# Kernel tuning notes

Measured on AMD Instinct MI355X. Metric: run time of the kernel, lower is better.

Reference implementation:

```python
import jax, jax.numpy as jnp
import numpy as np

DIM_IN, DIM_Q, DIM_K = 1024, 128, 128
B, S = 8, 2048

def setup_inputs() -> dict:
    key = jax.random.key(0)
    ks = jax.random.split(key, 9)
    sq = 1.0 / np.sqrt(DIM_IN)
    return {
        "query": jax.random.normal(ks[0], (B, S, DIM_IN), jnp.float32),
        "key": jax.random.normal(ks[1], (B, S, DIM_IN), jnp.float32),
        "value": jax.random.normal(ks[2], (B, S, DIM_IN), jnp.float32),
        "Wq": jax.random.uniform(ks[3], (DIM_IN, DIM_Q), jnp.float32, -sq, sq),
        "bq": jax.random.uniform(ks[4], (DIM_Q,), jnp.float32, -sq, sq),
        "Wk": jax.random.uniform(ks[5], (DIM_IN, DIM_K), jnp.float32, -sq, sq),
        "bk": jax.random.uniform(ks[6], (DIM_K,), jnp.float32, -sq, sq),
        "Wv": jax.random.uniform(ks[7], (DIM_IN, DIM_K), jnp.float32, -sq, sq),
        "bv": jax.random.uniform(ks[8], (DIM_K,), jnp.float32, -sq, sq),
    }

def reference(query, key, value, Wq, bq, Wk, bk, Wv, bv):
    q = jnp.einsum("bsd,dq->bsq", query, Wq) + bq          # [B,S,Dq]
    k = jnp.einsum("bsd,dk->bsk", key, Wk) + bk            # [B,S,Dk]
    v = jnp.einsum("bsd,dk->bsk", value, Wv) + bv          # [B,S,Dk]
    scale = jnp.asarray(q.shape[-1] ** 0.5, q.dtype)
    scores = jnp.einsum("bqd,bkd->bqk", q, k) / scale      # [B,S,S]
    attn = jax.nn.softmax(scores, axis=-1)
    return jnp.einsum("bqk,bkd->bqd", attn, v)             # [B,S,Dk]
```

## Files before the change

### kernel.cpp

```cpp
#include <hip/hip_runtime.h>

typedef __attribute__((ext_vector_type(8))) short short8;
typedef __attribute__((ext_vector_type(4))) float floatx4;

#define MFMA16(a, b, c) __builtin_amdgcn_mfma_f32_16x16x32_bf16(a, b, c, 0, 0, 0)

__device__ __forceinline__ short f2bf(float f) {
    unsigned int u = __float_as_uint(f);
    u = u + 0x7fffu + ((u >> 16) & 1u);
    return (short)(u >> 16);
}

__device__ __forceinline__ void ldst16(const void* g, void* l) {
    __builtin_amdgcn_global_load_lds(
        (const __attribute__((address_space(1))) void*)g,
        (__attribute__((address_space(3))) void*)l, 16, 0, 0);
}

__global__ __launch_bounds__(256) void wconv_kernel(const float* __restrict__ Wq,
                                                    const float* __restrict__ Wk,
                                                    const float* __restrict__ Wv,
                                                    short* __restrict__ wt) {
    int idx = blockIdx.x * 256 + threadIdx.x;
    int w = idx >> 17;
    int rem = idx & 131071;
    int k = rem >> 7, n = rem & 127;
    const float* W = (w == 0) ? Wq : (w == 1) ? Wk : Wv;
    wt[w * 131072 + n * 1024 + k] = f2bf(W[rem]);
}

__global__ __launch_bounds__(256, 3) void proj_kernel(const float* __restrict__ Q,
                                                      const float* __restrict__ K,
                                                      const float* __restrict__ V,
                                                      const short* __restrict__ wt,
                                                      const float* __restrict__ bq,
                                                      const float* __restrict__ bk,
                                                      const float* __restrict__ bv,
                                                      short* __restrict__ qo,
                                                      short* __restrict__ ko,
                                                      short* __restrict__ vo) {
    alignas(16) __shared__ float Asl[64 * 64];
    alignas(16) __shared__ short Wsl[128 * 64];
    const int t = threadIdx.x;
    const int wv = t >> 6, L = t & 63;
    const int q4 = L >> 4, l16 = L & 15;
    const int which = blockIdx.y;
    const float* A = (which == 0) ? Q : (which == 1) ? K : V;
    const short* Wt = wt + which * 131072;
    const float* bias = (which == 0) ? bq : (which == 1) ? bk : bv;
    const int m0 = blockIdx.x * 64;
    const int mw = m0 + 16 * wv;

    floatx4 acc[8];
    for (int nt = 0; nt < 8; nt++) acc[nt] = (floatx4)0.0f;

    for (int k0 = 0; k0 < 1024; k0 += 64) {
        __syncthreads();
        for (int j = 0; j < 4; j++) {
            int s = (4 * wv + j) * 64 + L;
            int r = s >> 4, p = s & 15, c = p ^ (r & 15);
            ldst16(A + (size_t)(m0 + r) * 1024 + k0 + c * 4,
                   Asl + (4 * wv + j) * 256);
        }
        for (int j = 0; j < 4; j++) {
            int s = (4 * wv + j) * 64 + L;
            int r = s >> 3, p = s & 7, c = p ^ (r & 7);
            ldst16(Wt + (size_t)r * 1024 + k0 + c * 8,
                   Wsl + (4 * wv + j) * 512);
        }
        __syncthreads();

        for (int ks = 0; ks < 2; ks++) {
            int c0 = 8 * ks + 2 * q4;
            const int ar = 16 * wv + l16;
            float4 f0 = *(float4*)&Asl[ar * 64 + (c0 ^ l16) * 4];
            float4 f1 = *(float4*)&Asl[ar * 64 + ((c0 + 1) ^ l16) * 4];
            short8 af;
            af[0] = f2bf(f0.x); af[1] = f2bf(f0.y); af[2] = f2bf(f0.z); af[3] = f2bf(f0.w);
            af[4] = f2bf(f1.x); af[5] = f2bf(f1.y); af[6] = f2bf(f1.z); af[7] = f2bf(f1.w);
            int cw = 4 * ks + q4;
            for (int nt = 0; nt < 8; nt++) {
                int wr = 16 * nt + l16;
                short8 bf = *(short8*)&Wsl[wr * 64 + (cw ^ (l16 & 7)) * 8];
                acc[nt] = MFMA16(af, bf, acc[nt]);
            }
        }
    }

    for (int nt = 0; nt < 8; nt++) {
        float bvv = bias[16 * nt + l16];
        for (int r = 0; r < 4; r++) {
            float val = acc[nt][r] + bvv;
            short h = f2bf(val);
            int grow = mw + q4 * 4 + r;
            int col = 16 * nt + l16;
            if (which == 0) {
                qo[(size_t)grow * 128 + col] = h;
            } else if (which == 1) {
                ko[(size_t)grow * 128 + col] = h;
            } else {
                int bb = grow >> 11, s = grow & 2047;
                vo[(size_t)bb * 262144 + (size_t)col * 2048 + s] = h;
            }
        }
    }
}

__global__ __launch_bounds__(256, 2) void flash_kernel(const short* __restrict__ qw,
                                                       const short* __restrict__ kw,
                                                       const short* __restrict__ vw,
                                                       float* __restrict__ out) {
    alignas(16) __shared__ short Kl[2][64][136];
    alignas(16) __shared__ short Vl[2][128][72];
    alignas(16) __shared__ short Pl[2][32][72];
    const int t = threadIdx.x;
    const int wv = t >> 6, L = t & 63;
    const int pr = wv >> 1, wq = wv & 1;
    const int pt = t & 127;
    const int q4 = L >> 4, l16 = L & 15;
    const int bq = blockIdx.x, b = blockIdx.y;
    const short* qp = qw + (size_t)b * 262144 + (size_t)bq * 32 * 128;
    const short* kp = kw + (size_t)b * 262144;
    const short* vp = vw + (size_t)b * 262144;

    short8 qf[4];
    for (int ks = 0; ks < 4; ks++)
        qf[ks] = *(const short8*)(qp + (16 * wq + l16) * 128 + ks * 32 + q4 * 8);

    floatx4 oacc[8];
    for (int dt = 0; dt < 8; dt++) oacc[dt] = (floatx4)0.0f;
    float m_i[4] = {-1e30f, -1e30f, -1e30f, -1e30f};
    float l_i[4] = {0.f, 0.f, 0.f, 0.f};
    const float SL = (float)(0.08838834764831845 * 1.4426950408889634);

    for (int kt = 0; kt < 16; kt++) {
        const int kv0 = (pr * 16 + kt) * 64;
        __syncthreads();
        for (int j = 0; j < 8; j++) {
            int flat = j * 128 + pt;
            int row = flat >> 4, c16 = flat & 15;
            *(short8*)&Kl[pr][row][c16 * 8] = *(const short8*)(kp + (size_t)(kv0 + row) * 128 + c16 * 8);
        }
        for (int j = 0; j < 8; j++) {
            int flat = j * 128 + pt;
            int row = flat >> 3, c8 = flat & 7;
            *(short8*)&Vl[pr][row][c8 * 8] = *(const short8*)(vp + (size_t)row * 2048 + kv0 + c8 * 8);
        }
        __syncthreads();

        floatx4 sa[4];
        for (int nt = 0; nt < 4; nt++) {
            sa[nt] = (floatx4)0.0f;
            for (int ks = 0; ks < 4; ks++) {
                short8 bfr = *(short8*)&Kl[pr][16 * nt + l16][ks * 32 + q4 * 8];
                sa[nt] = MFMA16(qf[ks], bfr, sa[nt]);
            }
        }

        float p[4][4], mnew[4], alpha[4];
        for (int r = 0; r < 4; r++) {
            float mx = fmaxf(fmaxf(sa[0][r], sa[1][r]), fmaxf(sa[2][r], sa[3][r]));
            mx *= SL;
            for (int off = 8; off >= 1; off >>= 1) mx = fmaxf(mx, __shfl_xor(mx, off, 64));
            mnew[r] = fmaxf(m_i[r], mx);
            alpha[r] = __builtin_amdgcn_exp2f(m_i[r] - mnew[r]);
            float rs = 0.f;
            for (int nt = 0; nt < 4; nt++) {
                float pv = __builtin_amdgcn_exp2f(sa[nt][r] * SL - mnew[r]);
                p[nt][r] = pv;
                rs += pv;
            }
            for (int off = 8; off >= 1; off >>= 1) rs += __shfl_xor(rs, off, 64);
            l_i[r] = l_i[r] * alpha[r] + rs;
            m_i[r] = mnew[r];
        }
        for (int dt = 0; dt < 8; dt++)
            for (int r = 0; r < 4; r++) oacc[dt][r] *= alpha[r];

        for (int nt = 0; nt < 4; nt++)
            for (int r = 0; r < 4; r++)
                Pl[pr][16 * wq + q4 * 4 + r][16 * nt + l16] = f2bf(p[nt][r]);

        short8 pf0 = *(short8*)&Pl[pr][16 * wq + l16][q4 * 8];
        short8 pf1 = *(short8*)&Pl[pr][16 * wq + l16][32 + q4 * 8];
        for (int dt = 0; dt < 8; dt++) {
            short8 v0 = *(short8*)&Vl[pr][16 * dt + l16][q4 * 8];
            short8 v1 = *(short8*)&Vl[pr][16 * dt + l16][32 + q4 * 8];
            oacc[dt] = MFMA16(pf0, v0, oacc[dt]);
            oacc[dt] = MFMA16(pf1, v1, oacc[dt]);
        }
    }

    __syncthreads();
    float* Om = (float*)&Kl[0][0][0];
    float* Mm = (float*)&Vl[0][0][0];
    float* Lm = Mm + 64;
    if (pr == 1) {
        for (int dt = 0; dt < 8; dt++)
            for (int r = 0; r < 4; r++)
                Om[(16 * wq + q4 * 4 + r) * 128 + 16 * dt + l16] = oacc[dt][r];
        if (l16 == 0)
            for (int r = 0; r < 4; r++) {
                Mm[16 * wq + q4 * 4 + r] = m_i[r];
                Lm[16 * wq + q4 * 4 + r] = l_i[r];
            }
    }
    __syncthreads();
    if (pr == 0) {
        float s0[4], s1[4];
        for (int r = 0; r < 4; r++) {
            int row = 16 * wq + q4 * 4 + r;
            float m1 = Mm[row], l1 = Lm[row];
            float M = fmaxf(m_i[r], m1);
            float a0 = __builtin_amdgcn_exp2f(m_i[r] - M);
            float a1 = __builtin_amdgcn_exp2f(m1 - M);
            float inv = 1.0f / (l_i[r] * a0 + l1 * a1);
            s0[r] = a0 * inv; s1[r] = a1 * inv;
        }
        for (int dt = 0; dt < 8; dt++) {
            for (int r = 0; r < 4; r++) {
                int row = 16 * wq + q4 * 4 + r;
                int qrow = bq * 32 + row;
                out[((size_t)b * 2048 + qrow) * 128 + 16 * dt + l16] =
                    oacc[dt][r] * s0[r] + Om[row * 128 + 16 * dt + l16] * s1[r];
            }
        }
    }
}

extern "C" void kernel_launch(void* const* d_in, const int* in_sizes, int n_in,
                              void* d_out, int out_size, void* d_ws, size_t ws_size,
                              hipStream_t stream) {
    const float* query = (const float*)d_in[0];
    const float* key   = (const float*)d_in[1];
    const float* value = (const float*)d_in[2];
    const float* Wq    = (const float*)d_in[3];
    const float* bq    = (const float*)d_in[4];
    const float* Wk    = (const float*)d_in[5];
    const float* bk    = (const float*)d_in[6];
    const float* Wv    = (const float*)d_in[7];
    const float* bv    = (const float*)d_in[8];
    float* out = (float*)d_out;

    short* wt  = (short*)d_ws;
    short* qws = wt + 3 * 131072;
    short* kws = qws + 16384 * 128;
    short* vws = kws + 16384 * 128;

    wconv_kernel<<<1536, 256, 0, stream>>>(Wq, Wk, Wv, wt);
    proj_kernel<<<dim3(256, 3), 256, 0, stream>>>(query, key, value, wt,
                                                  bq, bk, bv, qws, kws, vws);
    flash_kernel<<<dim3(64, 8), 256, 0, stream>>>(qws, kws, vws, out);
}
```

Before: 280.3 us.

## Double-buffer projection tiles and use direct-to-LDS swizzled loads in flash kernel

The projection kernel now double-buffers its A and W LDS tiles, so the next k-slice is issued with global_load_lds while the current one feeds MFMAs. Occupancy drops from 3 to 2 blocks per CU to make room for the doubled LDS. The flash kernel swaps padded register-staged K/V copies for direct global-to-LDS loads into XOR-swizzled layouts, which cuts VGPR traffic and keeps reads free of bank conflicts. The risks are lower occupancy in the projection kernel and the async LDS loads still sitting behind a sync in the flash loop.

```diff
diff --git a/kernel.cpp b/kernel.cpp
--- a/kernel.cpp
+++ b/kernel.cpp
@@ -29,7 +29,7 @@
     wt[w * 131072 + n * 1024 + k] = f2bf(W[rem]);
 }
 
-__global__ __launch_bounds__(256, 3) void proj_kernel(const float* __restrict__ Q,
+__global__ __launch_bounds__(256, 2) void proj_kernel(const float* __restrict__ Q,
                                                       const float* __restrict__ K,
                                                       const float* __restrict__ V,
                                                       const short* __restrict__ wt,
@@ -39,8 +39,8 @@
                                                       short* __restrict__ qo,
                                                       short* __restrict__ ko,
                                                       short* __restrict__ vo) {
-    alignas(16) __shared__ float Asl[64 * 64];
-    alignas(16) __shared__ short Wsl[128 * 64];
+    alignas(16) __shared__ float Asl[2][64 * 64];
+    alignas(16) __shared__ short Wsl[2][128 * 64];
     const int t = threadIdx.x;
     const int wv = t >> 6, L = t & 63;
     const int q4 = L >> 4, l16 = L & 15;
@@ -54,37 +54,42 @@
     floatx4 acc[8];
     for (int nt = 0; nt < 8; nt++) acc[nt] = (floatx4)0.0f;
 
-    for (int k0 = 0; k0 < 1024; k0 += 64) {
-        __syncthreads();
+    auto stage = [&](int buf, int k0) {
         for (int j = 0; j < 4; j++) {
             int s = (4 * wv + j) * 64 + L;
-            int r = s >> 4, p = s & 15, c = p ^ (r & 15);
+            int r = s >> 4, c = (s & 15) ^ (r & 15);
             ldst16(A + (size_t)(m0 + r) * 1024 + k0 + c * 4,
-                   Asl + (4 * wv + j) * 256);
+                   &Asl[buf][(4 * wv + j) * 256]);
         }
         for (int j = 0; j < 4; j++) {
             int s = (4 * wv + j) * 64 + L;
-            int r = s >> 3, p = s & 7, c = p ^ (r & 7);
+            int r = s >> 3, c = (s & 7) ^ (r & 7);
             ldst16(Wt + (size_t)r * 1024 + k0 + c * 8,
-                   Wsl + (4 * wv + j) * 512);
-        }
+                   &Wsl[buf][(4 * wv + j) * 512]);
+        }
+    };
+
+    stage(0, 0);
+    int p = 0;
+    for (int kt = 0; kt < 16; kt++) {
         __syncthreads();
-
+        if (kt < 15) stage(p ^ 1, (kt + 1) * 64);
         for (int ks = 0; ks < 2; ks++) {
             int c0 = 8 * ks + 2 * q4;
             const int ar = 16 * wv + l16;
-            float4 f0 = *(float4*)&Asl[ar * 64 + (c0 ^ l16) * 4];
-            float4 f1 = *(float4*)&Asl[ar * 64 + ((c0 + 1) ^ l16) * 4];
+            float4 f0 = *(float4*)&Asl[p][ar * 64 + (c0 ^ l16) * 4];
+            float4 f1 = *(float4*)&Asl[p][ar * 64 + ((c0 + 1) ^ l16) * 4];
             short8 af;
             af[0] = f2bf(f0.x); af[1] = f2bf(f0.y); af[2] = f2bf(f0.z); af[3] = f2bf(f0.w);
             af[4] = f2bf(f1.x); af[5] = f2bf(f1.y); af[6] = f2bf(f1.z); af[7] = f2bf(f1.w);
             int cw = 4 * ks + q4;
             for (int nt = 0; nt < 8; nt++) {
                 int wr = 16 * nt + l16;
-                short8 bf = *(short8*)&Wsl[wr * 64 + (cw ^ (l16 & 7)) * 8];
+                short8 bf = *(short8*)&Wsl[p][wr * 64 + (cw ^ (l16 & 7)) * 8];
                 acc[nt] = MFMA16(af, bf, acc[nt]);
             }
         }
+        p ^= 1;
     }
 
     for (int nt = 0; nt < 8; nt++) {
@@ -110,13 +115,12 @@
                                                        const short* __restrict__ kw,
                                                        const short* __restrict__ vw,
                                                        float* __restrict__ out) {
-    alignas(16) __shared__ short Kl[2][64][136];
-    alignas(16) __shared__ short Vl[2][128][72];
+    alignas(16) __shared__ short Kls[2][64 * 128];
+    alignas(16) __shared__ short Vls[2][128 * 64];
     alignas(16) __shared__ short Pl[2][32][72];
     const int t = threadIdx.x;
-    const int wv = t >> 6, L = t & 63;
-    const int pr = wv >> 1, wq = wv & 1;
-    const int pt = t & 127;
+    const int wvi = t >> 6, L = t & 63;
+    const int pr = wvi >> 1, wq = wvi & 1;
     const int q4 = L >> 4, l16 = L & 15;
     const int bq = blockIdx.x, b = blockIdx.y;
     const short* qp = qw + (size_t)b * 262144 + (size_t)bq * 32 * 128;
@@ -137,14 +141,16 @@
         const int kv0 = (pr * 16 + kt) * 64;
         __syncthreads();
         for (int j = 0; j < 8; j++) {
-            int flat = j * 128 + pt;
-            int row = flat >> 4, c16 = flat & 15;
-            *(short8*)&Kl[pr][row][c16 * 8] = *(const short8*)(kp + (size_t)(kv0 + row) * 128 + c16 * 8);
+            int sb = (8 * wq + j) * 64;
+            int s = sb + L;
+            int r = s >> 4, c = (s & 15) ^ (r & 15);
+            ldst16(kp + (size_t)(kv0 + r) * 128 + c * 8, &Kls[pr][sb * 8]);
         }
         for (int j = 0; j < 8; j++) {
-            int flat = j * 128 + pt;
-            int row = flat >> 3, c8 = flat & 7;
-            *(short8*)&Vl[pr][row][c8 * 8] = *(const short8*)(vp + (size_t)row * 2048 + kv0 + c8 * 8);
+            int sb = (8 * wq + j) * 64;
+            int s = sb + L;
+            int r = s >> 3, c = (s & 7) ^ (r & 7);
+            ldst16(vp + (size_t)r * 2048 + kv0 + c * 8, &Vls[pr][sb * 8]);
         }
         __syncthreads();
 
@@ -152,7 +158,7 @@
         for (int nt = 0; nt < 4; nt++) {
             sa[nt] = (floatx4)0.0f;
             for (int ks = 0; ks < 4; ks++) {
-                short8 bfr = *(short8*)&Kl[pr][16 * nt + l16][ks * 32 + q4 * 8];
+                short8 bfr = *(short8*)&Kls[pr][(16 * nt + l16) * 128 + ((4 * ks + q4) ^ l16) * 8];
                 sa[nt] = MFMA16(qf[ks], bfr, sa[nt]);
             }
         }
@@ -184,16 +190,16 @@
         short8 pf0 = *(short8*)&Pl[pr][16 * wq + l16][q4 * 8];
         short8 pf1 = *(short8*)&Pl[pr][16 * wq + l16][32 + q4 * 8];
         for (int dt = 0; dt < 8; dt++) {
-            short8 v0 = *(short8*)&Vl[pr][16 * dt + l16][q4 * 8];
-            short8 v1 = *(short8*)&Vl[pr][16 * dt + l16][32 + q4 * 8];
+            short8 v0 = *(short8*)&Vls[pr][(16 * dt + l16) * 64 + (q4 ^ (l16 & 7)) * 8];
+            short8 v1 = *(short8*)&Vls[pr][(16 * dt + l16) * 64 + ((4 + q4) ^ (l16 & 7)) * 8];
             oacc[dt] = MFMA16(pf0, v0, oacc[dt]);
             oacc[dt] = MFMA16(pf1, v1, oacc[dt]);
         }
     }
 
     __syncthreads();
-    float* Om = (float*)&Kl[0][0][0];
-    float* Mm = (float*)&Vl[0][0][0];
+    float* Om = (float*)&Kls[0][0];
+    float* Mm = (float*)&Vls[0][0];
     float* Lm = Mm + 64;
     if (pr == 1) {
         for (int dt = 0; dt < 8; dt++)
```

Measured after the change: 292.6 us. 1.04x slower.
